# Optimization experiments

Hardware: AMD Instinct MI355X
Metric: run time of the kernel (lower is better)

## Reference

```python
import jax, jax.numpy as jnp
import numpy as np

MIN_SCALE = 0.05
MAX_SCALE = 0.2
EPS = 0.001
RATE = 4
SUBSAMPLE = 3


def box_filter(x, k):
    # matches torch: pad (1+p) before / p after on H and W, double cumsum + subtract
    if k % 2 == 0:
        k = k + 1
    p = k // 2
    xp = jnp.pad(x, ((0, 0), (0, 0), (1 + p, p), (1 + p, p)))
    c = jnp.cumsum(xp, axis=2)
    y = c[:, :, k:, :] - c[:, :, :-k, :]
    c2 = jnp.cumsum(y, axis=3)
    return c2[:, :, :, k:] - c2[:, :, :, :-k]


def _resize(x, h, w):
    # torch F.interpolate(mode='bilinear', align_corners=False) == jax bilinear, no antialias
    n, c = x.shape[0], x.shape[1]
    return jax.image.resize(x, (n, c, h, w), method='bilinear', antialias=False)


def rf_norm(x):
    N, C, H, W = x.shape
    scale = MAX_SCALE
    it = 1
    while True:  # loop bounds depend only on static config -> Python loop is jit-safe
        win = int(max(H, W) * scale)
        if win < 3 and it == 1:
            mean = x.mean(axis=(1, 2, 3), keepdims=True)
            std = x.std(axis=(1, 2, 3), ddof=1, keepdims=True) + EPS
            x = x / std - mean / std
        else:
            if SUBSAMPLE > 1 and min(H, W) > SUBSAMPLE * 10 and win > SUBSAMPLE * 5:
                xs = _resize(x, H // SUBSAMPLE, W // SUBSAMPLE)
                win = win // SUBSAMPLE
            else:
                xs = x
            h, w = xs.shape[2], xs.shape[3]
            ones = jnp.ones((1, 1, h, w), x.dtype)
            M = box_filter(ones, win)
            x_mean = box_filter(xs, win).mean(axis=1, keepdims=True) / M
            x2_mean = box_filter(xs ** 2, win).mean(axis=1, keepdims=True) / M
            var = jnp.clip(x2_mean - x_mean ** 2, 0.0) + EPS
            std = jnp.sqrt(var)
            a = 1.0 / std
            b = -x_mean / std
            mean_a = box_filter(a, win) / M
            mean_b = box_filter(b, win) / M
            if SUBSAMPLE > 1:
                mean_a = _resize(mean_a, H, W)
                mean_b = _resize(mean_b, H, W)
            x = mean_a * x + mean_b
        it += 1
        scale /= RATE  # coarse_to_fine=True
        if scale < MIN_SCALE:
            break
    return x


def setup_inputs() -> dict:
    key = jax.random.key(0)
    x = jax.random.normal(key, (16, 3, 768, 768), dtype=jnp.float32)
    return {"x": x}


def reference(x):
    return rf_norm(x)
```

## Files before the change

### kernel.cpp

```cpp
#include <hip/hip_runtime.h>


#define N_B 16
#define CCH 3
#define HF 768
#define HL 256
#define SLICE (HL * HL)
#define TOT_L (N_B * SLICE)
#define EPSV 1e-3f

__device__ __forceinline__ int cnt(int i, int P) {
  int hi = i + P; if (hi > HL - 1) hi = HL - 1;
  int lo = i - P; if (lo < 0) lo = 0;
  return hi - lo + 1;
}

__device__ __forceinline__ void scan2g(float a, float b, int g, int j,
    float2 (*s)[HL], float2 (*wt)[4]) {
  int lane = j & 63, w = j >> 6;
#pragma unroll
  for (int d = 1; d < 64; d <<= 1) {
    float ta = __shfl_up(a, (unsigned)d);
    float tb = __shfl_up(b, (unsigned)d);
    if (lane >= d) { a += ta; b += tb; }
  }
  if (lane == 63) wt[g][w] = make_float2(a, b);
  __syncthreads();
  float offa = 0.f, offb = 0.f;
  for (int ww = 0; ww < w; ++ww) { float2 t = wt[g][ww]; offa += t.x; offb += t.y; }
  s[g][j] = make_float2(a + offa, b + offb);
  __syncthreads();
}

template <int P>
__device__ __forceinline__ float2 boxr(const float2 (*s)[HL], int g, int j) {
  int hi = j + P; if (hi > HL - 1) hi = HL - 1;
  int lo = j - P - 1;
  float2 r = s[g][hi];
  if (lo >= 0) { float2 l = s[g][lo]; r.x -= l.x; r.y -= l.y; }
  return r;
}

template <int P>
__device__ __forceinline__ void xpose_store(const float2 (*s)[HL], int tid,
    float2* __restrict__ dst, size_t nb, int col0) {
  if (tid < HL) {
    float2 r0 = boxr<P>(s, 0, tid);
    float2 r1 = boxr<P>(s, 1, tid);
    float2 r2 = boxr<P>(s, 2, tid);
    float2 r3 = boxr<P>(s, 3, tid);
    float4* d = (float4*)(dst + nb + (size_t)tid * HL + col0);
    d[0] = make_float4(r0.x, r0.y, r1.x, r1.y);
    d[1] = make_float4(r2.x, r2.y, r3.x, r3.y);
  }
}

__global__ __launch_bounds__(1024) void k1(const float* __restrict__ x,
    float2* __restrict__ UV, float2* __restrict__ Spk) {
  __shared__ float2 sA[4][HL];
  __shared__ float2 wtA[4][4];
  int b = blockIdx.x;
  int n = b >> 6;
  int ib = (b & 63) << 2;
  int tid = threadIdx.x;
  int g = tid >> 8, j = tid & 255;
  const float* xp = x + (size_t)n * CCH * HF * HF
                  + (size_t)(3 * (ib + g) + 1) * HF + (3 * j + 1);
  float c0 = xp[0], c1 = xp[HF * HF], c2 = xp[2 * HF * HF];
  float uu = (c0 + c1 + c2) * (1.f / 3.f);
  float vv = (c0 * c0 + c1 * c1 + c2 * c2) * (1.f / 3.f);
  size_t nb = (size_t)n * SLICE;
  UV[nb + (size_t)(ib + g) * HL + j] = make_float2(uu, vv);
  scan2g(uu, vv, g, j, sA, wtA);
  xpose_store<25>(sA, tid, Spk, nb, ib);
}

__global__ __launch_bounds__(1024) void k2(const float2* __restrict__ Spk,
    float2* __restrict__ Ppk) {
  __shared__ float2 sA[4][HL], sB[4][HL];
  __shared__ float2 wtA[4][4], wtB[4][4];
  int n = blockIdx.x >> 6, strip = blockIdx.x & 63;
  int tid = threadIdx.x, g = tid >> 8, j = tid & 255;
  int c = strip * 4 + g;
  size_t nb = (size_t)n * SLICE;
  float2 sv = Spk[nb + (size_t)c * HL + j];
  scan2g(sv.x, sv.y, g, j, sA, wtA);
  float2 bu = boxr<25>(sA, g, j);
  float invM = 1.f / ((float)cnt(j, 25) * (float)cnt(c, 25));
  float xm = bu.x * invM, x2m = bu.y * invM;
  float var = x2m - xm * xm; if (var < 0.f) var = 0.f;
  float inv = 1.f / sqrtf(var + EPSV);
  scan2g(inv, -xm * inv, g, j, sB, wtB);
  xpose_store<25>(sB, tid, Ppk, nb, strip * 4);
}

__global__ __launch_bounds__(1024) void k3(const float2* __restrict__ Ppk,
    const float2* __restrict__ UV, float2* __restrict__ AB1,
    float2* __restrict__ Qpk) {
  __shared__ float2 sA[4][HL], sB[4][HL];
  __shared__ float2 wtA[4][4], wtB[4][4];
  int n = blockIdx.x >> 6, strip = blockIdx.x & 63;
  int tid = threadIdx.x, g = tid >> 8, j = tid & 255;
  int i = strip * 4 + g;
  size_t nb = (size_t)n * SLICE;
  size_t idx = nb + (size_t)i * HL + j;
  float2 pv = Ppk[idx];
  scan2g(pv.x, pv.y, g, j, sA, wtA);
  float2 bb = boxr<25>(sA, g, j);
  float invM = 1.f / ((float)cnt(i, 25) * (float)cnt(j, 25));
  float Av = bb.x * invM, Bv = bb.y * invM;
  AB1[idx] = make_float2(Av, Bv);
  float2 uv = UV[idx];
  float u2 = Av * uv.x + Bv;
  float v2 = Av * Av * uv.y + 2.f * Av * Bv * uv.x + Bv * Bv;
  scan2g(u2, v2, g, j, sB, wtB);
  xpose_store<6>(sB, tid, Qpk, nb, strip * 4);
}

__global__ __launch_bounds__(1024) void k4(const float2* __restrict__ Qpk,
    float2* __restrict__ Rpk) {
  __shared__ float2 sA[4][HL], sB[4][HL];
  __shared__ float2 wtA[4][4], wtB[4][4];
  int n = blockIdx.x >> 6, strip = blockIdx.x & 63;
  int tid = threadIdx.x, g = tid >> 8, j = tid & 255;
  int c = strip * 4 + g;
  size_t nb = (size_t)n * SLICE;
  float2 qv = Qpk[nb + (size_t)c * HL + j];
  scan2g(qv.x, qv.y, g, j, sA, wtA);
  float2 bu = boxr<6>(sA, g, j);
  float invM = 1.f / ((float)cnt(j, 6) * (float)cnt(c, 6));
  float xm = bu.x * invM, x2m = bu.y * invM;
  float var = x2m - xm * xm; if (var < 0.f) var = 0.f;
  float inv = 1.f / sqrtf(var + EPSV);
  scan2g(inv, -xm * inv, g, j, sB, wtB);
  xpose_store<6>(sB, tid, Rpk, nb, strip * 4);
}

__device__ __forceinline__ void upw(int q, int& i0, int& i1, float& w1) {
  int d = q / 3;
  int r = q - 3 * d;
  if (r == 1) { i0 = d; i1 = d; w1 = 0.f; }
  else if (r == 2) { i0 = d; i1 = d + 1; if (i1 > HL - 1) i1 = HL - 1; w1 = 1.f / 3.f; }
  else { i1 = d; i0 = d - 1; if (i0 < 0) i0 = 0; w1 = 2.f / 3.f; }
}

__global__ __launch_bounds__(256) void k_final(
    const float* __restrict__ x, const float2* __restrict__ AB1,
    const float2* __restrict__ Rpk, float* __restrict__ out) {
  __shared__ float2 ry01[HL], ry23[HL];
  __shared__ float2 sA[1][HL], sB[1][HL];
  __shared__ float2 wtA[1][4], wtB[1][4];
  int nb_ = blockIdx.x;
  int y = nb_ % HF;
  int n = nb_ / HF;
  int t = threadIdx.x;
  int iy0, iy1;
  float wy1;
  upw(y, iy0, iy1, wy1);
  float wy0 = 1.f - wy1;
  size_t mb = (size_t)n * SLICE;
  float2 a0 = AB1[mb + (size_t)iy0 * HL + t];
  float2 a1 = AB1[mb + (size_t)iy1 * HL + t];
  ry01[t] = make_float2(wy0 * a0.x + wy1 * a1.x, wy0 * a0.y + wy1 * a1.y);
  float cj6 = (float)cnt(t, 6);
  float2 r0v = Rpk[mb + (size_t)iy0 * HL + t];
  scan2g(r0v.x, r0v.y, 0, t, sA, wtA);
  float2 b0 = boxr<6>(sA, 0, t);
  float inv0 = 1.f / ((float)cnt(iy0, 6) * cj6);
  float A20 = b0.x * inv0, B20 = b0.y * inv0;
  if (wy1 == 0.f) {
    ry23[t] = make_float2(A20, B20);
  } else {
    float2 r1v = Rpk[mb + (size_t)iy1 * HL + t];
    scan2g(r1v.x, r1v.y, 0, t, sB, wtB);
    float2 b1 = boxr<6>(sB, 0, t);
    float inv1 = 1.f / ((float)cnt(iy1, 6) * cj6);
    ry23[t] = make_float2(wy0 * A20 + wy1 * b1.x * inv1,
                          wy0 * B20 + wy1 * b1.y * inv1);
  }
  __syncthreads();
  if (t < 192) {
    float A1c[4], B1c[4], A2c[4], B2c[4];
#pragma unroll
    for (int e = 0; e < 4; ++e) {
      int q = 4 * t + e;
      int ix0, ix1;
      float wx1;
      upw(q, ix0, ix1, wx1);
      float wx0 = 1.f - wx1;
      float2 m0 = ry01[ix0], m1 = ry01[ix1];
      float2 m2 = ry23[ix0], m3 = ry23[ix1];
      A1c[e] = wx0 * m0.x + wx1 * m1.x;
      B1c[e] = wx0 * m0.y + wx1 * m1.y;
      A2c[e] = wx0 * m2.x + wx1 * m3.x;
      B2c[e] = wx0 * m2.y + wx1 * m3.y;
    }
    size_t rowbase = ((size_t)(n * CCH) * HF + y) * HF + 4 * t;
#pragma unroll
    for (int c = 0; c < CCH; ++c) {
      const float4 xin = *(const float4*)(x + rowbase + (size_t)c * HF * HF);
      float4 o;
      o.x = A2c[0] * (A1c[0] * xin.x + B1c[0]) + B2c[0];
      o.y = A2c[1] * (A1c[1] * xin.y + B1c[1]) + B2c[1];
      o.z = A2c[2] * (A1c[2] * xin.z + B1c[2]) + B2c[2];
      o.w = A2c[3] * (A1c[3] * xin.w + B1c[3]) + B2c[3];
      *(float4*)(out + rowbase + (size_t)c * HF * HF) = o;
    }
  }
}

extern "C" void kernel_launch(void* const* d_in, const int* in_sizes, int n_in,
                              void* d_out, int out_size, void* d_ws, size_t ws_size,
                              hipStream_t stream) {
  const float* x = (const float*)d_in[0];
  float* out = (float*)d_out;
  const size_t S = (size_t)TOT_L;
  float2 *UV, *Spk, *Ppk, *AB1, *Rpk, *Qpk;
  if (ws_size >= 10 * S * sizeof(float)) {
    float2* w = (float2*)d_ws;
    UV = w; Spk = UV + S; Ppk = Spk + S; AB1 = Ppk + S; Rpk = AB1 + S;
  } else {
    AB1 = (float2*)d_ws; Rpk = AB1 + S;
    UV = (float2*)out; Spk = UV + S; Ppk = Spk + S;
  }
  Qpk = Spk;

  k1<<<N_B * 64, 1024, 0, stream>>>(x, UV, Spk);
  k2<<<N_B * 64, 1024, 0, stream>>>(Spk, Ppk);
  k3<<<N_B * 64, 1024, 0, stream>>>(Ppk, UV, AB1, Qpk);
  k4<<<N_B * 64, 1024, 0, stream>>>(Qpk, Rpk);
  k_final<<<N_B * HF, 256, 0, stream>>>(x, AB1, Rpk, out);
}
```

Measured before the change: 96.19 us.

## Process three output rows per final block sharing scanned low-res rows

The final kernel now handles three full-resolution output rows per block (768 threads). It scans the three neighbouring low-res R rows once and shares them, where before each output row rescanned one or two rows itself, and the grid shrinks from 12288 to 4096 blocks. The transposed store in the scan kernels is also spread over 512 threads, each writing one float4 instead of two. The scan helper gains an unused template parameter. The cost is a larger block with more shared memory, which may lower occupancy in the final kernel.

```diff
diff --git a/kernel.cpp b/kernel.cpp
--- a/kernel.cpp
+++ b/kernel.cpp
@@ -15,6 +15,7 @@
   return hi - lo + 1;
 }
 
+template <int G>
 __device__ __forceinline__ void scan2g(float a, float b, int g, int j,
     float2 (*s)[HL], float2 (*wt)[4]) {
   int lane = j & 63, w = j >> 6;
@@ -44,14 +45,12 @@
 template <int P>
 __device__ __forceinline__ void xpose_store(const float2 (*s)[HL], int tid,
     float2* __restrict__ dst, size_t nb, int col0) {
-  if (tid < HL) {
-    float2 r0 = boxr<P>(s, 0, tid);
-    float2 r1 = boxr<P>(s, 1, tid);
-    float2 r2 = boxr<P>(s, 2, tid);
-    float2 r3 = boxr<P>(s, 3, tid);
-    float4* d = (float4*)(dst + nb + (size_t)tid * HL + col0);
-    d[0] = make_float4(r0.x, r0.y, r1.x, r1.y);
-    d[1] = make_float4(r2.x, r2.y, r3.x, r3.y);
+  if (tid < 512) {
+    int row = tid & 255, half = tid >> 8;
+    float2 r0 = boxr<P>(s, 2 * half, row);
+    float2 r1 = boxr<P>(s, 2 * half + 1, row);
+    float4* d = (float4*)(dst + nb + (size_t)row * HL + col0);
+    d[half] = make_float4(r0.x, r0.y, r1.x, r1.y);
   }
 }
 
@@ -71,7 +70,7 @@
   float vv = (c0 * c0 + c1 * c1 + c2 * c2) * (1.f / 3.f);
   size_t nb = (size_t)n * SLICE;
   UV[nb + (size_t)(ib + g) * HL + j] = make_float2(uu, vv);
-  scan2g(uu, vv, g, j, sA, wtA);
+  scan2g<4>(uu, vv, g, j, sA, wtA);
   xpose_store<25>(sA, tid, Spk, nb, ib);
 }
 
@@ -84,13 +83,13 @@
   int c = strip * 4 + g;
   size_t nb = (size_t)n * SLICE;
   float2 sv = Spk[nb + (size_t)c * HL + j];
-  scan2g(sv.x, sv.y, g, j, sA, wtA);
+  scan2g<4>(sv.x, sv.y, g, j, sA, wtA);
   float2 bu = boxr<25>(sA, g, j);
   float invM = 1.f / ((float)cnt(j, 25) * (float)cnt(c, 25));
   float xm = bu.x * invM, x2m = bu.y * invM;
   float var = x2m - xm * xm; if (var < 0.f) var = 0.f;
   float inv = 1.f / sqrtf(var + EPSV);
-  scan2g(inv, -xm * inv, g, j, sB, wtB);
+  scan2g<4>(inv, -xm * inv, g, j, sB, wtB);
   xpose_store<25>(sB, tid, Ppk, nb, strip * 4);
 }
 
@@ -105,7 +104,7 @@
   size_t nb = (size_t)n * SLICE;
   size_t idx = nb + (size_t)i * HL + j;
   float2 pv = Ppk[idx];
-  scan2g(pv.x, pv.y, g, j, sA, wtA);
+  scan2g<4>(pv.x, pv.y, g, j, sA, wtA);
   float2 bb = boxr<25>(sA, g, j);
   float invM = 1.f / ((float)cnt(i, 25) * (float)cnt(j, 25));
   float Av = bb.x * invM, Bv = bb.y * invM;
@@ -113,7 +112,7 @@
   float2 uv = UV[idx];
   float u2 = Av * uv.x + Bv;
   float v2 = Av * Av * uv.y + 2.f * Av * Bv * uv.x + Bv * Bv;
-  scan2g(u2, v2, g, j, sB, wtB);
+  scan2g<4>(u2, v2, g, j, sB, wtB);
   xpose_store<6>(sB, tid, Qpk, nb, strip * 4);
 }
 
@@ -126,13 +125,13 @@
   int c = strip * 4 + g;
   size_t nb = (size_t)n * SLICE;
   float2 qv = Qpk[nb + (size_t)c * HL + j];
-  scan2g(qv.x, qv.y, g, j, sA, wtA);
+  scan2g<4>(qv.x, qv.y, g, j, sA, wtA);
   float2 bu = boxr<6>(sA, g, j);
   float invM = 1.f / ((float)cnt(j, 6) * (float)cnt(c, 6));
   float xm = bu.x * invM, x2m = bu.y * invM;
   float var = x2m - xm * xm; if (var < 0.f) var = 0.f;
   float inv = 1.f / sqrtf(var + EPSV);
-  scan2g(inv, -xm * inv, g, j, sB, wtB);
+  scan2g<4>(inv, -xm * inv, g, j, sB, wtB);
   xpose_store<6>(sB, tid, Rpk, nb, strip * 4);
 }
 
@@ -144,58 +143,54 @@
   else { i1 = d; i0 = d - 1; if (i0 < 0) i0 = 0; w1 = 2.f / 3.f; }
 }
 
-__global__ __launch_bounds__(256) void k_final(
+__global__ __launch_bounds__(768) void k_final(
     const float* __restrict__ x, const float2* __restrict__ AB1,
     const float2* __restrict__ Rpk, float* __restrict__ out) {
-  __shared__ float2 ry01[HL], ry23[HL];
-  __shared__ float2 sA[1][HL], sB[1][HL];
-  __shared__ float2 wtA[1][4], wtB[1][4];
+  __shared__ float2 s[3][HL];
+  __shared__ float2 wt[3][4];
+  __shared__ float2 ry01[3][HL], ry23[3][HL];
   int nb_ = blockIdx.x;
-  int y = nb_ % HF;
-  int n = nb_ / HF;
-  int t = threadIdx.x;
-  int iy0, iy1;
-  float wy1;
-  upw(y, iy0, iy1, wy1);
+  int d = nb_ & 255, n = nb_ >> 8;
+  int tid = threadIdx.x, g = tid >> 8, j = tid & 255;
+  size_t mb = (size_t)n * SLICE;
+  int rg = d - 1 + g; rg = rg < 0 ? 0 : (rg > HL - 1 ? HL - 1 : rg);
+  float2 rv = Rpk[mb + (size_t)rg * HL + j];
+  scan2g<3>(rv.x, rv.y, g, j, s, wt);
+  int s0 = (g == 0) ? 0 : 1;
+  int s1 = (g == 2) ? 2 : 1;
+  float wy1 = (g == 0) ? (2.f / 3.f) : ((g == 2) ? (1.f / 3.f) : 0.f);
   float wy0 = 1.f - wy1;
-  size_t mb = (size_t)n * SLICE;
-  float2 a0 = AB1[mb + (size_t)iy0 * HL + t];
-  float2 a1 = AB1[mb + (size_t)iy1 * HL + t];
-  ry01[t] = make_float2(wy0 * a0.x + wy1 * a1.x, wy0 * a0.y + wy1 * a1.y);
-  float cj6 = (float)cnt(t, 6);
-  float2 r0v = Rpk[mb + (size_t)iy0 * HL + t];
-  scan2g(r0v.x, r0v.y, 0, t, sA, wtA);
-  float2 b0 = boxr<6>(sA, 0, t);
-  float inv0 = 1.f / ((float)cnt(iy0, 6) * cj6);
-  float A20 = b0.x * inv0, B20 = b0.y * inv0;
-  if (wy1 == 0.f) {
-    ry23[t] = make_float2(A20, B20);
-  } else {
-    float2 r1v = Rpk[mb + (size_t)iy1 * HL + t];
-    scan2g(r1v.x, r1v.y, 0, t, sB, wtB);
-    float2 b1 = boxr<6>(sB, 0, t);
-    float inv1 = 1.f / ((float)cnt(iy1, 6) * cj6);
-    ry23[t] = make_float2(wy0 * A20 + wy1 * b1.x * inv1,
-                          wy0 * B20 + wy1 * b1.y * inv1);
-  }
+  int r0 = d - 1 + s0; r0 = r0 < 0 ? 0 : (r0 > HL - 1 ? HL - 1 : r0);
+  int r1 = d - 1 + s1; r1 = r1 < 0 ? 0 : (r1 > HL - 1 ? HL - 1 : r1);
+  float cj6 = (float)cnt(j, 6);
+  float2 b0 = boxr<6>(s, s0, j);
+  float2 b1 = boxr<6>(s, s1, j);
+  float i0f = 1.f / ((float)cnt(r0, 6) * cj6);
+  float i1f = 1.f / ((float)cnt(r1, 6) * cj6);
+  ry23[g][j] = make_float2(wy0 * b0.x * i0f + wy1 * b1.x * i1f,
+                           wy0 * b0.y * i0f + wy1 * b1.y * i1f);
+  float2 a0 = AB1[mb + (size_t)r0 * HL + j];
+  float2 a1 = AB1[mb + (size_t)r1 * HL + j];
+  ry01[g][j] = make_float2(wy0 * a0.x + wy1 * a1.x, wy0 * a0.y + wy1 * a1.y);
   __syncthreads();
-  if (t < 192) {
+  if (j < 192) {
+    int y = 3 * d + g;
     float A1c[4], B1c[4], A2c[4], B2c[4];
 #pragma unroll
     for (int e = 0; e < 4; ++e) {
-      int q = 4 * t + e;
+      int q = 4 * j + e;
       int ix0, ix1;
       float wx1;
       upw(q, ix0, ix1, wx1);
       float wx0 = 1.f - wx1;
-      float2 m0 = ry01[ix0], m1 = ry01[ix1];
-      float2 m2 = ry23[ix0], m3 = ry23[ix1];
+      float2 m0 = ry01[g][ix0], m1 = ry01[g][ix1];
+      float2 m2 = ry23[g][ix0], m3 = ry23[g][ix1];
       A1c[e] = wx0 * m0.x + wx1 * m1.x;
       B1c[e] = wx0 * m0.y + wx1 * m1.y;
       A2c[e] = wx0 * m2.x + wx1 * m3.x;
       B2c[e] = wx0 * m2.y + wx1 * m3.y;
     }
-    size_t rowbase = ((size_t)(n * CCH) * HF + y) * HF + 4 * t;
+    size_t rowbase = ((size_t)(n * CCH) * HF + y) * HF + 4 * j;
 #pragma unroll
     for (int c = 0; c < CCH; ++c) {
       const float4 xin = *(const float4*)(x + rowbase + (size_t)c * HF * HF);
@@ -229,5 +224,5 @@
   k2<<<N_B * 64, 1024, 0, stream>>>(Spk, Ppk);
   k3<<<N_B * 64, 1024, 0, stream>>>(Ppk, UV, AB1, Qpk);
   k4<<<N_B * 64, 1024, 0, stream>>>(Qpk, Rpk);
-  k_final<<<N_B * HF, 256, 0, stream>>>(x, AB1, Rpk, out);
-}
+  k_final<<<N_B * HL, 768, 0, stream>>>(x, AB1, Rpk, out);
+}
```

Result: slower. 98.50 us (+2.4%).
